# Performance work log

Hardware: AMD Instinct MI355X
Metric: run time of the kernel (lower is better)

The kernel has to match this reference:

```python
import jax, jax.numpy as jnp
import numpy as np

B, H, W, C = 32, 56, 56, 192
P, HEADS = 7, 6
HD = C // HEADS
SCALE = HD ** -0.5
EPS = 1e-5


def _rel_pos_index(p):
    coords = np.stack(np.meshgrid(np.arange(p), np.arange(p), indexing='ij')).reshape(2, -1)
    rel = (coords[:, :, None] - coords[:, None, :]).transpose(1, 2, 0).astype(np.int64)
    rel[:, :, 0] += p - 1
    rel[:, :, 1] += p - 1
    rel[:, :, 0] *= 2 * p - 1
    return rel.sum(-1)  # (p*p, p*p)

REL_IDX = jnp.asarray(_rel_pos_index(P))


def _ln(x, g, b):
    mu = x.mean(-1, keepdims=True)
    var = ((x - mu) ** 2).mean(-1, keepdims=True)
    return (x - mu) * jax.lax.rsqrt(var + EPS) * g + b


def setup_inputs():
    key = jax.random.key(0)
    ks = jax.random.split(key, 8)
    s = 0.02
    return {
        'x': jax.random.normal(ks[0], (B, H * W, C), jnp.float32),
        'norm1_g': jnp.ones((C,), jnp.float32),
        'norm1_b': jnp.zeros((C,), jnp.float32),
        'qkv_w': jax.random.normal(ks[1], (C, 3 * C), jnp.float32) * s,
        'qkv_b': jnp.zeros((3 * C,), jnp.float32),
        'rpe_table': jax.random.normal(ks[2], ((2 * P - 1) ** 2, HEADS), jnp.float32) * s,
        'proj_w': jax.random.normal(ks[3], (C, C), jnp.float32) * s,
        'proj_b': jnp.zeros((C,), jnp.float32),
        'norm2_g': jnp.ones((C,), jnp.float32),
        'norm2_b': jnp.zeros((C,), jnp.float32),
        'fc1_w': jax.random.normal(ks[4], (C, 4 * C), jnp.float32) * s,
        'fc1_b': jnp.zeros((4 * C,), jnp.float32),
        'fc2_w': jax.random.normal(ks[5], (4 * C, C), jnp.float32) * s,
        'fc2_b': jnp.zeros((C,), jnp.float32),
    }


def reference(x, norm1_g, norm1_b, qkv_w, qkv_b, rpe_table, proj_w, proj_b,
              norm2_g, norm2_b, fc1_w, fc1_b, fc2_w, fc2_b):
    N = P * P
    shortcut = x
    h = _ln(x, norm1_g, norm1_b).reshape(B, H, W, C)
    # partition -> (B*nH*nW, N, C)
    h = h.reshape(B, H // P, P, W // P, P, C).transpose(0, 1, 3, 2, 4, 5)
    patches = h.reshape(-1, N, C)
    B_ = patches.shape[0]
    # qkv
    qkv = (patches @ qkv_w + qkv_b).reshape(B_, N, 3, HEADS, HD)
    q, k, v = qkv[:, :, 0], qkv[:, :, 1], qkv[:, :, 2]  # (B_, N, HEADS, HD)
    attn = jnp.einsum('bnhd,bmhd->bhnm', q * SCALE, k)
    bias = rpe_table[REL_IDX.reshape(-1)].reshape(N, N, HEADS).transpose(2, 0, 1)
    attn = jax.nn.softmax(attn + bias[None], axis=-1)
    out = jnp.einsum('bhnm,bmhd->bnhd', attn, v).reshape(B_, N, C)
    out = out @ proj_w + proj_b
    # reverse -> (B, H*W, C)
    out = out.reshape(B, H // P, W // P, P, P, C).transpose(0, 1, 3, 2, 4, 5).reshape(B, H * W, C)
    x = shortcut + out
    h = _ln(x, norm2_g, norm2_b)
    h = jax.nn.gelu(h @ fc1_w + fc1_b, approximate=False) @ fc2_w + fc2_b
    return x + h
```

## Files before the change

### kernel.cpp

```cpp
#include <hip/hip_runtime.h>
#include <cstdint>

using u16 = unsigned short;
using u32 = unsigned int;

typedef __bf16 bf16x8 __attribute__((ext_vector_type(8)));
typedef float f32x4 __attribute__((ext_vector_type(4)));
typedef short short4v __attribute__((ext_vector_type(4)));

constexpr int TOK = 100352;
constexpr float LOG2E = 1.4426950408889634f;
constexpr float SCALE_QL = 0.25503490f;

__device__ __forceinline__ float bf2f(u16 u) {
  union { u32 i; float f; } z; z.i = ((u32)u) << 16; return z.f;
}
__device__ __forceinline__ u16 f2bf(float f) {
  union { float f; u32 i; } z; z.f = f;
  u32 r = z.i + 0x7FFFu + ((z.i >> 16) & 1u);
  return (u16)(r >> 16);
}
__device__ __forceinline__ u32 pk2bf(float a, float b) {
  union { __bf16 h[2]; u32 w; } z;
  z.h[0] = (__bf16)a; z.h[1] = (__bf16)b; return z.w;
}

__device__ __forceinline__ float gelu_f(float v) {
  float u = v * (0.7978845608f + 0.0356774081f * v * v);
  float e = __expf(-2.f * u);
  return v * __builtin_amdgcn_rcpf(1.f + e);
}

__device__ __forceinline__ void gload_lds16(const void* g, void* l) {
  __builtin_amdgcn_global_load_lds((const __attribute__((address_space(1))) void*)g,
                                   (__attribute__((address_space(3))) void*)l, 16, 0, 0);
}

__global__ void transpose_pad(const float* __restrict__ src, u16* __restrict__ dst,
                              int N, int Npad, int K) {
  int id = blockIdx.x * 256 + threadIdx.x;
  if (id >= Npad * K) return;
  int n = id / K, k = id - n * K;
  float v = (n < N) ? src[(size_t)k * N + n] : 0.f;
  dst[id] = f2bf(v);
}

__global__ void transpose_swz1(const float* __restrict__ src, u16* __restrict__ dst) {
  int id = blockIdx.x * 256 + threadIdx.x;
  if (id >= 768 * 192) return;
  int n = id / 192, k = id - n * 192;
  int sg = (k >> 3) ^ (n & 7);
  dst[n * 192 + sg * 8 + (k & 7)] = f2bf(src[(size_t)k * 768 + n]);
}
__global__ void transpose_swz2(const float* __restrict__ src, u16* __restrict__ dst) {
  int id = blockIdx.x * 256 + threadIdx.x;
  if (id >= 192 * 768) return;
  int oc = id / 768, gc = id - oc * 768;
  int ch = gc >> 5, gcl = gc & 31;
  int f = gcl >> 4, gq = (gcl >> 2) & 3, e = gcl & 3;
  int P = oc * 4 + (gq ^ ((oc >> 2) & 3));
  dst[ch * 6144 + P * 8 + f * 4 + e] = f2bf(src[(size_t)gc * 192 + oc]);
}

template<int MODE>
__global__ __launch_bounds__(256) void ln_kernel(const float* __restrict__ x,
                                                 const u16* __restrict__ proj,
                                                 const float* __restrict__ g,
                                                 const float* __restrict__ b,
                                                 u16* __restrict__ out) {
  int row  = blockIdx.x * 4 + (threadIdx.x >> 6);
  int lane = threadIdx.x & 63;
  const float* xr = x + (size_t)row * 192;
  float v[3];
  #pragma unroll
  for (int t = 0; t < 3; ++t) {
    int c = lane + 64 * t;
    v[t] = xr[c];
    if (MODE == 1) v[t] += bf2f(proj[(size_t)row * 192 + c]);
  }
  float s = v[0] + v[1] + v[2];
  #pragma unroll
  for (int o = 32; o; o >>= 1) s += __shfl_xor(s, o);
  float mu = s * (1.f / 192.f);
  float q = 0.f;
  #pragma unroll
  for (int t = 0; t < 3; ++t) { float d = v[t] - mu; q += d * d; }
  #pragma unroll
  for (int o = 32; o; o >>= 1) q += __shfl_xor(q, o);
  float rs = rsqrtf(q * (1.f / 192.f) + 1e-5f);
  #pragma unroll
  for (int t = 0; t < 3; ++t) {
    int c = lane + 64 * t;
    out[(size_t)row * 192 + c] = f2bf((v[t] - mu) * rs * g[c] + b[c]);
  }
}

enum { MQKV = 0, MPROJ = 1 };

template<int MODE, int MT, int NT, int N, int K, int LDC>
__global__ __launch_bounds__(256) void gemm_kernel(
    const u16* __restrict__ A, const u16* __restrict__ BT,
    const float* __restrict__ bias,
    u16* __restrict__ outb)
{
  constexpr int NWG = MT * NT;
  constexpr int NTL = K / 32;
  __shared__ __align__(16) u16 As[3][4096];
  __shared__ __align__(16) u16 Bs[3][4096];
  int tid = threadIdx.x;
  int wg = blockIdx.x;
  int lin = (wg & 7) * (NWG / 8) + (wg >> 3);
  int tileM = (lin / NT) * 128, tileN = (lin % NT) * 128;
  int lane = tid & 63, wave = tid >> 6;
  int wm = wave >> 1, wn = wave & 1;
  int g = lane >> 4, l15 = lane & 15;
  f32x4 acc[4][4] = {};

  int r0 = tid >> 2, kc = (tid & 3) * 8;
  const u16* Arow0 = A  + (size_t)(tileM + r0)      * K + kc;
  const u16* Arow1 = A  + (size_t)(tileM + r0 + 64) * K + kc;
  const u16* Brow0 = BT + (size_t)(tileN + r0)      * K + kc;
  const u16* Brow1 = BT + (size_t)(tileN + r0 + 64) * K + kc;
  const int wo = wave * 512;

#define GSTAGE(buf, k0) do {                              \
    gload_lds16(Arow0 + (k0), &As[buf][wo]);              \
    gload_lds16(Arow1 + (k0), &As[buf][2048 + wo]);       \
    gload_lds16(Brow0 + (k0), &Bs[buf][wo]);              \
    gload_lds16(Brow1 + (k0), &Bs[buf][2048 + wo]);       \
  } while (0)

  GSTAGE(0, 0);
  GSTAGE(1, 32);

  #pragma unroll
  for (int t = 0; t < NTL; ++t) {
    if (t + 1 < NTL) asm volatile("s_waitcnt vmcnt(4)" ::: "memory");
    else             asm volatile("s_waitcnt vmcnt(0)" ::: "memory");
    __builtin_amdgcn_s_barrier();
    __builtin_amdgcn_sched_barrier(0);
    if (t + 2 < NTL) GSTAGE((t + 2) % 3, (t + 2) * 32);
    const int cur = t % 3;
    bf16x8 af[4], bfr[4];
    #pragma unroll
    for (int mi = 0; mi < 4; ++mi)
      af[mi] = *(const bf16x8*)&As[cur][(wm * 64 + mi * 16 + l15) * 32 + g * 8];
    #pragma unroll
    for (int ni = 0; ni < 4; ++ni)
      bfr[ni] = *(const bf16x8*)&Bs[cur][(wn * 64 + ni * 16 + l15) * 32 + g * 8];
    #pragma unroll
    for (int mi = 0; mi < 4; ++mi)
      #pragma unroll
      for (int ni = 0; ni < 4; ++ni)
        acc[mi][ni] = __builtin_amdgcn_mfma_f32_16x16x32_bf16(bfr[ni], af[mi], acc[mi][ni], 0, 0, 0);
    __builtin_amdgcn_sched_barrier(0);
  }
#undef GSTAGE

  int cb = tileN + wn * 64 + g * 4;
  f32x4 bv4[4];
  bool cok[4];
  #pragma unroll
  for (int ni = 0; ni < 4; ++ni) {
    cok[ni] = (cb + ni * 16) < N;
    bv4[ni] = cok[ni] ? *(const f32x4*)&bias[cb + ni * 16] : f32x4{};
  }
  #pragma unroll
  for (int mi = 0; mi < 4; ++mi) {
    size_t row = (size_t)(tileM + wm * 64 + mi * 16 + l15);
    u16* orow = outb + row * LDC + cb;
    #pragma unroll
    for (int ni = 0; ni < 4; ++ni) {
      if (!cok[ni]) continue;
      float v0 = acc[mi][ni][0] + bv4[ni][0];
      float v1 = acc[mi][ni][1] + bv4[ni][1];
      float v2 = acc[mi][ni][2] + bv4[ni][2];
      float v3 = acc[mi][ni][3] + bv4[ni][3];
      if (MODE == MQKV && (cb + ni * 16) < 192) {
        v0 *= SCALE_QL; v1 *= SCALE_QL; v2 *= SCALE_QL; v3 *= SCALE_QL;
      }
      uint2 w;
      w.x = pk2bf(v0, v1);
      w.y = pk2bf(v2, v3);
      *(uint2*)&orow[ni * 16] = w;
    }
  }
}

__global__ __launch_bounds__(256, 3) void mlp_fused(
    const u16* __restrict__ h2, const float* __restrict__ x,
    const u16* __restrict__ projO,
    const u16* __restrict__ w1g,
    const u16* __restrict__ w2g,
    const float* __restrict__ fc1b, const float* __restrict__ fc2b,
    float* __restrict__ out)
{
  __shared__ __align__(16) u16 W1c[2][6144];
  __shared__ __align__(16) u16 W2c[2][6144];
  __shared__ float B1s[768];
  __shared__ float B2s[192];

  int tid = threadIdx.x, lane = tid & 63, wave = tid >> 6;
  int g = lane >> 4, l15 = lane & 15;
  size_t row = (size_t)blockIdx.x * 64 + wave * 16 + l15;

  for (int c = tid; c < 768; c += 256) B1s[c] = fc1b[c];
  if (tid < 192) B2s[tid] = fc2b[tid];

  bf16x8 xf[6];
  #pragma unroll
  for (int ks = 0; ks < 6; ++ks)
    xf[ks] = *(const bf16x8*)&h2[row * 192 + ks * 32 + g * 8];

#define MSTAGE(c) do {                                                    \
    _Pragma("unroll")                                                     \
    for (int it = 0; it < 3; ++it) {                                      \
      int s = it * 256 + tid;                                             \
      gload_lds16(w1g + (size_t)(c) * 6144 + s * 8,                       \
                  &W1c[(c) & 1][(it * 256 + wave * 64) * 8]);             \
      gload_lds16(w2g + (size_t)(c) * 6144 + s * 8,                       \
                  &W2c[(c) & 1][(it * 256 + wave * 64) * 8]);             \
    }                                                                     \
  } while (0)

  MSTAGE(0);
  __syncthreads();

  f32x4 accO[12] = {};
  const int p2sw = g ^ ((l15 >> 2) & 3);

  #pragma unroll 2
  for (int c = 0; c < 24; ++c) {
    asm volatile("s_waitcnt vmcnt(0)" ::: "memory");
    __builtin_amdgcn_s_barrier();
    __builtin_amdgcn_sched_barrier(0);
    if (c + 1 < 24) MSTAGE(c + 1);
    const int bs = c & 1;

    f32x4 acc1[2] = {};
    #pragma unroll
    for (int ks = 0; ks < 6; ++ks) {
      #pragma unroll
      for (int f = 0; f < 2; ++f) {
        int rl = f * 16 + l15;
        int sg = (ks * 4 + g) ^ (rl & 7);
        bf16x8 wf = *(const bf16x8*)&W1c[bs][rl * 192 + sg * 8];
        acc1[f] = __builtin_amdgcn_mfma_f32_16x16x32_bf16(wf, xf[ks], acc1[f], 0, 0, 0);
      }
    }
    short4v bp[2];
    #pragma unroll
    for (int f = 0; f < 2; ++f) {
      f32x4 bv = *(const f32x4*)&B1s[c * 32 + f * 16 + g * 4];
      float p0 = gelu_f(acc1[f][0] + bv[0]);
      float p1 = gelu_f(acc1[f][1] + bv[1]);
      float p2 = gelu_f(acc1[f][2] + bv[2]);
      float p3 = gelu_f(acc1[f][3] + bv[3]);
      union { u32 w[2]; short4v v; } uu;
      uu.w[0] = pk2bf(p0, p1);
      uu.w[1] = pk2bf(p2, p3);
      bp[f] = uu.v;
    }
    #pragma unroll
    for (int n = 0; n < 12; ++n) {
      int oc = n * 16 + l15;
      int P = oc * 4 + p2sw;
      union { bf16x8 v8; short4v h[2]; } wu;
      wu.v8 = *(const bf16x8*)&W2c[bs][P * 8];
      accO[n] = __builtin_amdgcn_mfma_f32_16x16x16bf16_1k(wu.h[0], bp[0], accO[n], 0, 0, 0);
      accO[n] = __builtin_amdgcn_mfma_f32_16x16x16bf16_1k(wu.h[1], bp[1], accO[n], 0, 0, 0);
    }
    __builtin_amdgcn_sched_barrier(0);
  }
#undef MSTAGE

  const float* xrow = x + row * 192;
  const u16*  prow = projO + row * 192;
  float*      orow = out + row * 192;
  #pragma unroll
  for (int n = 0; n < 12; ++n) {
    int cb = n * 16 + g * 4;
    f32x4 bv = *(const f32x4*)&B2s[cb];
    f32x4 xv = *(const f32x4*)&xrow[cb];
    uint2 pv = *(const uint2*)&prow[cb];
    f32x4 o;
    o[0] = accO[n][0] + bv[0] + xv[0] + bf2f((u16)(pv.x & 0xffff));
    o[1] = accO[n][1] + bv[1] + xv[1] + bf2f((u16)(pv.x >> 16));
    o[2] = accO[n][2] + bv[2] + xv[2] + bf2f((u16)(pv.y & 0xffff));
    o[3] = accO[n][3] + bv[3] + xv[3] + bf2f((u16)(pv.y >> 16));
    *(f32x4*)&orow[cb] = o;
  }
}

__global__ __launch_bounds__(384, 4) void attn_kernel(const u16* __restrict__ qkv,
                                                      const float* __restrict__ rpe,
                                                      u16* __restrict__ aout) {
  __shared__ __align__(16) u16 VT[192 * 72];
  __shared__ float RPE[1014];

  int tid = threadIdx.x;
  int win = blockIdx.x;
  int b = win >> 6, rem = win & 63, wh = rem >> 3, ww = rem & 7;
  const size_t wbase = (size_t)b * 3136 + (size_t)(wh * 7) * 56 + ww * 7;

  for (int c = tid; c < 1176; c += 384) {
    int dchunk = c / 49, tkn = c - dchunk * 49;
    int d0 = dchunk * 8;
    int yi = tkn / 7, xi = tkn - yi * 7;
    size_t t = wbase + yi * 56 + xi;
    uint4 v = *(const uint4*)&qkv[t * 576 + 384 + d0];
    const u16* e = (const u16*)&v;
    #pragma unroll
    for (int u = 0; u < 8; ++u) VT[(d0 + u) * 72 + tkn] = e[u];
  }
  for (int c = tid; c < 2880; c += 384) {
    int d = c / 15, n = 49 + (c - d * 15);
    VT[d * 72 + n] = 0;
  }
  for (int c = tid; c < 1014; c += 384) RPE[c] = rpe[c] * LOG2E;
  __syncthreads();

  int wave = tid >> 6, lane = tid & 63;
  int g = lane >> 4, l15 = lane & 15;
  int h = wave;

  bf16x8 afk[4], bfq[4];
  #pragma unroll
  for (int f = 0; f < 4; ++f) {
    int row = f * 16 + l15; row = min(row, 48);
    int y = row / 7, xx = row - y * 7;
    const u16* base = &qkv[(wbase + (size_t)y * 56 + xx) * 576];
    bfq[f] = *(const bf16x8*)(base + h * 32 + g * 8);
    afk[f] = *(const bf16x8*)(base + 192 + h * 32 + g * 8);
  }

  f32x4 acc[4][4] = {};
  __builtin_amdgcn_s_setprio(1);
  #pragma unroll
  for (int mj = 0; mj < 4; ++mj)
    #pragma unroll
    for (int ni = 0; ni < 4; ++ni)
      acc[mj][ni] = __builtin_amdgcn_mfma_f32_16x16x32_bf16(afk[mj], bfq[ni], acc[mj][ni], 0, 0, 0);
  __builtin_amdgcn_s_setprio(0);

  float sums[4];
  short4v bp[4][4];
  #pragma unroll
  for (int ni = 0; ni < 4; ++ni) {
    int i = ni * 16 + l15;
    int yi = i / 7, xi = i - yi * 7;
    #pragma unroll
    for (int mj = 0; mj < 4; ++mj)
      #pragma unroll
      for (int r = 0; r < 4; ++r) {
        int j = mj * 16 + g * 4 + r;
        int yj = j / 7, xj = j - yj * 7;
        int idx = (yi - yj + 6) * 13 + (xi - xj + 6);
        idx = max(0, min(idx, 168));
        float s = acc[mj][ni][r] + RPE[idx * 6 + h];
        acc[mj][ni][r] = (j < 49) ? s : -1e30f;
      }
    float m = -1e30f;
    #pragma unroll
    for (int mj = 0; mj < 4; ++mj) {
      f32x4 a = acc[mj][ni];
      m = fmaxf(m, fmaxf(fmaxf(a[0], a[1]), fmaxf(a[2], a[3])));
    }
    m = fmaxf(m, __shfl_xor(m, 16));
    m = fmaxf(m, __shfl_xor(m, 32));
    float sum = 0.f;
    #pragma unroll
    for (int mj = 0; mj < 4; ++mj) {
      float p0 = exp2f(acc[mj][ni][0] - m);
      float p1 = exp2f(acc[mj][ni][1] - m);
      float p2 = exp2f(acc[mj][ni][2] - m);
      float p3 = exp2f(acc[mj][ni][3] - m);
      sum += (p0 + p1) + (p2 + p3);
      union { u32 w[2]; short4v v; } uu;
      uu.w[0] = pk2bf(p0, p1);
      uu.w[1] = pk2bf(p2, p3);
      bp[ni][mj] = uu.v;
    }
    sum += __shfl_xor(sum, 16);
    sum += __shfl_xor(sum, 32);
    sums[ni] = sum;
  }

  f32x4 accO[2][4] = {};
  #pragma unroll
  for (int ks = 0; ks < 4; ++ks) {
    short4v av[2];
    #pragma unroll
    for (int md = 0; md < 2; ++md)
      av[md] = *(const short4v*)&VT[(h * 32 + md * 16 + l15) * 72 + ks * 16 + g * 4];
    __builtin_amdgcn_s_setprio(1);
    #pragma unroll
    for (int md = 0; md < 2; ++md)
      #pragma unroll
      for (int ni = 0; ni < 4; ++ni)
        accO[md][ni] = __builtin_amdgcn_mfma_f32_16x16x16bf16_1k(av[md], bp[ni][ks], accO[md][ni], 0, 0, 0);
    __builtin_amdgcn_s_setprio(0);
  }

  #pragma unroll
  for (int ni = 0; ni < 4; ++ni) {
    int i = ni * 16 + l15;
    if (i >= 49) continue;
    float inv = __builtin_amdgcn_rcpf(sums[ni]);
    int y = i / 7, xx = i - y * 7;
    u16* orow = &aout[(wbase + (size_t)y * 56 + xx) * 192 + h * 32];
    #pragma unroll
    for (int md = 0; md < 2; ++md) {
      int d0 = md * 16 + g * 4;
      *(u32*)&orow[d0]     = pk2bf(accO[md][ni][0] * inv, accO[md][ni][1] * inv);
      *(u32*)&orow[d0 + 2] = pk2bf(accO[md][ni][2] * inv, accO[md][ni][3] * inv);
    }
  }
}

extern "C" void kernel_launch(void* const* d_in, const int* in_sizes, int n_in,
                              void* d_out, int out_size, void* d_ws, size_t ws_size,
                              hipStream_t stream) {
  const float* x      = (const float*)d_in[0];
  const float* n1g    = (const float*)d_in[1];
  const float* n1b    = (const float*)d_in[2];
  const float* qkv_w  = (const float*)d_in[3];
  const float* qkv_b  = (const float*)d_in[4];
  const float* rpe    = (const float*)d_in[5];
  const float* proj_w = (const float*)d_in[6];
  const float* proj_b = (const float*)d_in[7];
  const float* n2g    = (const float*)d_in[8];
  const float* n2b    = (const float*)d_in[9];
  const float* fc1_w  = (const float*)d_in[10];
  const float* fc1_b  = (const float*)d_in[11];
  const float* fc2_w  = (const float*)d_in[12];
  const float* fc2_b  = (const float*)d_in[13];
  float* out = (float*)d_out;
  char* ws = (char*)d_ws;

  u16* qkvT  = (u16*)(ws + 0);
  u16* projT = (u16*)(ws + 245760);
  u16* fc1T  = (u16*)(ws + 344064);
  u16* fc2T  = (u16*)(ws + 638976);
  u16* ln1   = (u16*)(ws + 1048576);
  u16* qkvB  = (u16*)(ws + 39583744);
  u16* projO = (u16*)(ws + 155189248);
  u16* attnO = ln1;
  u16* h2    = qkvB;
  if (ws_size < 193724416u) return;

  transpose_pad<<<(640*192+255)/256, 256, 0, stream>>>(qkv_w,  qkvT, 576, 640, 192);
  transpose_pad<<<(256*192+255)/256, 256, 0, stream>>>(proj_w, projT, 192, 256, 192);
  transpose_swz1<<<576, 256, 0, stream>>>(fc1_w, fc1T);
  transpose_swz2<<<576, 256, 0, stream>>>(fc2_w, fc2T);

  ln_kernel<0><<<TOK/4, 256, 0, stream>>>(x, nullptr, n1g, n1b, ln1);

  gemm_kernel<MQKV, 784, 5, 576, 192, 576><<<3920, 256, 0, stream>>>(
      ln1, qkvT, qkv_b, qkvB);

  attn_kernel<<<2048, 384, 0, stream>>>(qkvB, rpe, attnO);

  gemm_kernel<MPROJ, 784, 2, 192, 192, 192><<<1568, 256, 0, stream>>>(
      attnO, projT, proj_b, projO);

  ln_kernel<1><<<TOK/4, 256, 0, stream>>>(x, projO, n2g, n2b, h2);

  mlp_fused<<<TOK/64, 256, 0, stream>>>(
      h2, x, projO, fc1T, fc2T, fc1_b, fc2_b, out);
}
```

Baseline: 345.8 us.

## Double rows per wave in fused MLP to reuse staged weights; fold GELU into exp2

Each wave in the fused MLP kernel now processes two 16-row tiles, so every W1/W2 fragment read from LDS feeds two MFMAs. The grid is halved and launch bounds drop to 2 blocks per SM. The aim is to halve weight staging traffic and LDS reads per token. The cost is doubled accumulator registers and lower occupancy. GELU now folds the constants so it can call exp2f directly.

```diff
diff --git a/kernel.cpp b/kernel.cpp
--- a/kernel.cpp
+++ b/kernel.cpp
@@ -26,8 +26,8 @@
 }
 
 __device__ __forceinline__ float gelu_f(float v) {
-  float u = v * (0.7978845608f + 0.0356774081f * v * v);
-  float e = __expf(-2.f * u);
+  float t = -v * (2.3022587f + 0.10294455f * v * v);
+  float e = exp2f(t);
   return v * __builtin_amdgcn_rcpf(1.f + e);
 }
 
@@ -187,7 +187,7 @@
   }
 }
 
-__global__ __launch_bounds__(256, 3) void mlp_fused(
+__global__ __launch_bounds__(256, 2) void mlp_fused(
     const u16* __restrict__ h2, const float* __restrict__ x,
     const u16* __restrict__ projO,
     const u16* __restrict__ w1g,
@@ -202,15 +202,17 @@
 
   int tid = threadIdx.x, lane = tid & 63, wave = tid >> 6;
   int g = lane >> 4, l15 = lane & 15;
-  size_t row = (size_t)blockIdx.x * 64 + wave * 16 + l15;
+  size_t rowA = (size_t)blockIdx.x * 128 + wave * 32 + l15;
 
   for (int c = tid; c < 768; c += 256) B1s[c] = fc1b[c];
   if (tid < 192) B2s[tid] = fc2b[tid];
 
-  bf16x8 xf[6];
-  #pragma unroll
-  for (int ks = 0; ks < 6; ++ks)
-    xf[ks] = *(const bf16x8*)&h2[row * 192 + ks * 32 + g * 8];
+  bf16x8 xfA[6], xfB[6];
+  #pragma unroll
+  for (int ks = 0; ks < 6; ++ks) {
+    xfA[ks] = *(const bf16x8*)&h2[rowA * 192 + ks * 32 + g * 8];
+    xfB[ks] = *(const bf16x8*)&h2[(rowA + 16) * 192 + ks * 32 + g * 8];
+  }
 
 #define MSTAGE(c) do {                                                    \
     _Pragma("unroll")                                                     \
@@ -226,7 +228,8 @@
   MSTAGE(0);
   __syncthreads();
 
-  f32x4 accO[12] = {};
+  f32x4 accOA[12] = {};
+  f32x4 accOB[12] = {};
   const int p2sw = g ^ ((l15 >> 2) & 3);
 
   #pragma unroll 2
@@ -237,7 +240,7 @@
     if (c + 1 < 24) MSTAGE(c + 1);
     const int bs = c & 1;
 
-    f32x4 acc1[2] = {};
+    f32x4 acc1A[2] = {}, acc1B[2] = {};
     #pragma unroll
     for (int ks = 0; ks < 6; ++ks) {
       #pragma unroll
@@ -245,21 +248,34 @@
         int rl = f * 16 + l15;
         int sg = (ks * 4 + g) ^ (rl & 7);
         bf16x8 wf = *(const bf16x8*)&W1c[bs][rl * 192 + sg * 8];
-        acc1[f] = __builtin_amdgcn_mfma_f32_16x16x32_bf16(wf, xf[ks], acc1[f], 0, 0, 0);
+        acc1A[f] = __builtin_amdgcn_mfma_f32_16x16x32_bf16(wf, xfA[ks], acc1A[f], 0, 0, 0);
+        acc1B[f] = __builtin_amdgcn_mfma_f32_16x16x32_bf16(wf, xfB[ks], acc1B[f], 0, 0, 0);
       }
     }
-    short4v bp[2];
+    short4v bpA[2], bpB[2];
     #pragma unroll
     for (int f = 0; f < 2; ++f) {
       f32x4 bv = *(const f32x4*)&B1s[c * 32 + f * 16 + g * 4];
-      float p0 = gelu_f(acc1[f][0] + bv[0]);
-      float p1 = gelu_f(acc1[f][1] + bv[1]);
-      float p2 = gelu_f(acc1[f][2] + bv[2]);
-      float p3 = gelu_f(acc1[f][3] + bv[3]);
-      union { u32 w[2]; short4v v; } uu;
-      uu.w[0] = pk2bf(p0, p1);
-      uu.w[1] = pk2bf(p2, p3);
-      bp[f] = uu.v;
+      {
+        float p0 = gelu_f(acc1A[f][0] + bv[0]);
+        float p1 = gelu_f(acc1A[f][1] + bv[1]);
+        float p2 = gelu_f(acc1A[f][2] + bv[2]);
+        float p3 = gelu_f(acc1A[f][3] + bv[3]);
+        union { u32 w[2]; short4v v; } uu;
+        uu.w[0] = pk2bf(p0, p1);
+        uu.w[1] = pk2bf(p2, p3);
+        bpA[f] = uu.v;
+      }
+      {
+        float p0 = gelu_f(acc1B[f][0] + bv[0]);
+        float p1 = gelu_f(acc1B[f][1] + bv[1]);
+        float p2 = gelu_f(acc1B[f][2] + bv[2]);
+        float p3 = gelu_f(acc1B[f][3] + bv[3]);
+        union { u32 w[2]; short4v v; } uu;
+        uu.w[0] = pk2bf(p0, p1);
+        uu.w[1] = pk2bf(p2, p3);
+        bpB[f] = uu.v;
+      }
     }
     #pragma unroll
     for (int n = 0; n < 12; ++n) {
@@ -267,28 +283,35 @@
       int P = oc * 4 + p2sw;
       union { bf16x8 v8; short4v h[2]; } wu;
       wu.v8 = *(const bf16x8*)&W2c[bs][P * 8];
-      accO[n] = __builtin_amdgcn_mfma_f32_16x16x16bf16_1k(wu.h[0], bp[0], accO[n], 0, 0, 0);
-      accO[n] = __builtin_amdgcn_mfma_f32_16x16x16bf16_1k(wu.h[1], bp[1], accO[n], 0, 0, 0);
+      accOA[n] = __builtin_amdgcn_mfma_f32_16x16x16bf16_1k(wu.h[0], bpA[0], accOA[n], 0, 0, 0);
+      accOA[n] = __builtin_amdgcn_mfma_f32_16x16x16bf16_1k(wu.h[1], bpA[1], accOA[n], 0, 0, 0);
+      accOB[n] = __builtin_amdgcn_mfma_f32_16x16x16bf16_1k(wu.h[0], bpB[0], accOB[n], 0, 0, 0);
+      accOB[n] = __builtin_amdgcn_mfma_f32_16x16x16bf16_1k(wu.h[1], bpB[1], accOB[n], 0, 0, 0);
     }
     __builtin_amdgcn_sched_barrier(0);
   }
 #undef MSTAGE
 
-  const float* xrow = x + row * 192;
-  const u16*  prow = projO + row * 192;
-  float*      orow = out + row * 192;
-  #pragma unroll
-  for (int n = 0; n < 12; ++n) {
-    int cb = n * 16 + g * 4;
-    f32x4 bv = *(const f32x4*)&B2s[cb];
-    f32x4 xv = *(const f32x4*)&xrow[cb];
-    uint2 pv = *(const uint2*)&prow[cb];
-    f32x4 o;
-    o[0] = accO[n][0] + bv[0] + xv[0] + bf2f((u16)(pv.x & 0xffff));
-    o[1] = accO[n][1] + bv[1] + xv[1] + bf2f((u16)(pv.x >> 16));
-    o[2] = accO[n][2] + bv[2] + xv[2] + bf2f((u16)(pv.y & 0xffff));
-    o[3] = accO[n][3] + bv[3] + xv[3] + bf2f((u16)(pv.y >> 16));
-    *(f32x4*)&orow[cb] = o;
+  #pragma unroll
+  for (int half = 0; half < 2; ++half) {
+    size_t row = rowA + half * 16;
+    const f32x4* accO = half ? accOB : accOA;
+    const float* xrow = x + row * 192;
+    const u16*  prow = projO + row * 192;
+    float*      orow = out + row * 192;
+    #pragma unroll
+    for (int n = 0; n < 12; ++n) {
+      int cb = n * 16 + g * 4;
+      f32x4 bv = *(const f32x4*)&B2s[cb];
+      f32x4 xv = *(const f32x4*)&xrow[cb];
+      uint2 pv = *(const uint2*)&prow[cb];
+      f32x4 o;
+      o[0] = accO[n][0] + bv[0] + xv[0] + bf2f((u16)(pv.x & 0xffff));
+      o[1] = accO[n][1] + bv[1] + xv[1] + bf2f((u16)(pv.x >> 16));
+      o[2] = accO[n][2] + bv[2] + xv[2] + bf2f((u16)(pv.y & 0xffff));
+      o[3] = accO[n][3] + bv[3] + xv[3] + bf2f((u16)(pv.y >> 16));
+      *(f32x4*)&orow[cb] = o;
+    }
   }
 }
 
@@ -466,6 +489,6 @@
 
   ln_kernel<1><<<TOK/4, 256, 0, stream>>>(x, projO, n2g, n2b, h2);
 
-  mlp_fused<<<TOK/64, 256, 0, stream>>>(
+  mlp_fused<<<TOK/128, 256, 0, stream>>>(
       h2, x, projO, fc1T, fc2T, fc1_b, fc2_b, out);
 }
```

Measured after the change: 354.9 us. 1.03x slower.

## Fuse projection GEMM with residual add and LayerNorm2 into one kernel

Applied to the files above, without the earlier changes.

Replaces the separate projection GEMM and second LayerNorm kernels with one kernel. Each block computes a full 128x192 output row tile, adds bias and the residual, writes the fp32 residual, and computes LayerNorm statistics in registers before emitting bf16 h2. The MLP epilogue then reads the precomputed residual instead of x plus the bf16 projection output, which drops a launch and a round trip of the projection result. It also folds log2e into the GELU exponent so exp2f can be used. Risks are fewer workgroups (784) with high register pressure, and single-pass variance that is less numerically stable.

```diff
diff --git a/kernel.cpp b/kernel.cpp
--- a/kernel.cpp
+++ b/kernel.cpp
@@ -26,8 +26,8 @@
 }
 
 __device__ __forceinline__ float gelu_f(float v) {
-  float u = v * (0.7978845608f + 0.0356774081f * v * v);
-  float e = __expf(-2.f * u);
+  float t = -v * (2.3022587f + 0.10294455f * v * v);
+  float e = exp2f(t);
   return v * __builtin_amdgcn_rcpf(1.f + e);
 }
 
@@ -95,7 +95,7 @@
   }
 }
 
-enum { MQKV = 0, MPROJ = 1 };
+enum { MQKV = 0 };
 
 template<int MODE, int MT, int NT, int N, int K, int LDC>
 __global__ __launch_bounds__(256) void gemm_kernel(
@@ -187,9 +187,119 @@
   }
 }
 
+__global__ __launch_bounds__(256, 2) void proj_ln(
+    const u16* __restrict__ A,
+    const u16* __restrict__ BT,
+    const float* __restrict__ bias,
+    const float* __restrict__ x,
+    const float* __restrict__ n2g, const float* __restrict__ n2b,
+    float* __restrict__ resid, u16* __restrict__ h2)
+{
+  constexpr int NWG = 784;
+  __shared__ __align__(16) u16 As[3][4096];
+  __shared__ __align__(16) u16 Bs[3][6144];
+  int tid = threadIdx.x;
+  int wg = blockIdx.x;
+  int lin = (wg & 7) * (NWG / 8) + (wg >> 3);
+  int tileM = lin * 128;
+  int lane = tid & 63, wave = tid >> 6;
+  int g = lane >> 4, l15 = lane & 15;
+  f32x4 acc[2][12] = {};
+
+  int r0 = tid >> 2, kc = (tid & 3) * 8;
+  const u16* Arow0 = A + (size_t)(tileM + r0)      * 192 + kc;
+  const u16* Arow1 = A + (size_t)(tileM + r0 + 64) * 192 + kc;
+  const u16* Brow[3];
+  #pragma unroll
+  for (int i = 0; i < 3; ++i) {
+    int s = (wave * 3 + i) * 64 + lane;
+    Brow[i] = BT + (size_t)(s >> 2) * 192 + (s & 3) * 8;
+  }
+  const int wo = wave * 512;
+
+#define PSTAGE(buf, k0) do {                                   \
+    gload_lds16(Arow0 + (k0), &As[buf][wo]);                   \
+    gload_lds16(Arow1 + (k0), &As[buf][2048 + wo]);            \
+    _Pragma("unroll")                                          \
+    for (int i = 0; i < 3; ++i)                                \
+      gload_lds16(Brow[i] + (k0), &Bs[buf][(wave * 3 + i) * 512]); \
+  } while (0)
+
+  PSTAGE(0, 0);
+  PSTAGE(1, 32);
+
+  #pragma unroll
+  for (int t = 0; t < 6; ++t) {
+    if (t + 1 < 6) asm volatile("s_waitcnt vmcnt(5)" ::: "memory");
+    else           asm volatile("s_waitcnt vmcnt(0)" ::: "memory");
+    __builtin_amdgcn_s_barrier();
+    __builtin_amdgcn_sched_barrier(0);
+    if (t + 2 < 6) PSTAGE((t + 2) % 3, (t + 2) * 32);
+    const int cur = t % 3;
+    bf16x8 af[2], bfr[12];
+    #pragma unroll
+    for (int mi = 0; mi < 2; ++mi)
+      af[mi] = *(const bf16x8*)&As[cur][(wave * 32 + mi * 16 + l15) * 32 + g * 8];
+    #pragma unroll
+    for (int ni = 0; ni < 12; ++ni)
+      bfr[ni] = *(const bf16x8*)&Bs[cur][(ni * 16 + l15) * 32 + g * 8];
+    #pragma unroll
+    for (int mi = 0; mi < 2; ++mi)
+      #pragma unroll
+      for (int ni = 0; ni < 12; ++ni)
+        acc[mi][ni] = __builtin_amdgcn_mfma_f32_16x16x32_bf16(bfr[ni], af[mi], acc[mi][ni], 0, 0, 0);
+    __builtin_amdgcn_sched_barrier(0);
+  }
+#undef PSTAGE
+
+  float s1[2] = {0.f, 0.f}, s2[2] = {0.f, 0.f};
+  #pragma unroll
+  for (int mi = 0; mi < 2; ++mi) {
+    size_t row = (size_t)(tileM + wave * 32 + mi * 16 + l15);
+    #pragma unroll
+    for (int ni = 0; ni < 12; ++ni) {
+      int cb = ni * 16 + g * 4;
+      f32x4 bv = *(const f32x4*)&bias[cb];
+      f32x4 xv = *(const f32x4*)&x[row * 192 + cb];
+      f32x4 o;
+      #pragma unroll
+      for (int r = 0; r < 4; ++r) {
+        o[r] = acc[mi][ni][r] + bv[r] + xv[r];
+        s1[mi] += o[r];
+        s2[mi] += o[r] * o[r];
+      }
+      acc[mi][ni] = o;
+      *(f32x4*)&resid[row * 192 + cb] = o;
+    }
+  }
+  #pragma unroll
+  for (int mi = 0; mi < 2; ++mi) {
+    s1[mi] += __shfl_xor(s1[mi], 16); s1[mi] += __shfl_xor(s1[mi], 32);
+    s2[mi] += __shfl_xor(s2[mi], 16); s2[mi] += __shfl_xor(s2[mi], 32);
+  }
+  #pragma unroll
+  for (int mi = 0; mi < 2; ++mi) {
+    float mu = s1[mi] * (1.f / 192.f);
+    float var = s2[mi] * (1.f / 192.f) - mu * mu;
+    float rs = rsqrtf(var + 1e-5f);
+    size_t row = (size_t)(tileM + wave * 32 + mi * 16 + l15);
+    #pragma unroll
+    for (int ni = 0; ni < 12; ++ni) {
+      int cb = ni * 16 + g * 4;
+      f32x4 gv = *(const f32x4*)&n2g[cb];
+      f32x4 bv = *(const f32x4*)&n2b[cb];
+      uint2 w;
+      w.x = pk2bf((acc[mi][ni][0] - mu) * rs * gv[0] + bv[0],
+                  (acc[mi][ni][1] - mu) * rs * gv[1] + bv[1]);
+      w.y = pk2bf((acc[mi][ni][2] - mu) * rs * gv[2] + bv[2],
+                  (acc[mi][ni][3] - mu) * rs * gv[3] + bv[3]);
+      *(uint2*)&h2[row * 192 + cb] = w;
+    }
+  }
+}
+
 __global__ __launch_bounds__(256, 3) void mlp_fused(
-    const u16* __restrict__ h2, const float* __restrict__ x,
-    const u16* __restrict__ projO,
+    const u16* __restrict__ h2, const float* __restrict__ resid,
     const u16* __restrict__ w1g,
     const u16* __restrict__ w2g,
     const float* __restrict__ fc1b, const float* __restrict__ fc2b,
@@ -274,20 +384,18 @@
   }
 #undef MSTAGE
 
-  const float* xrow = x + row * 192;
-  const u16*  prow = projO + row * 192;
+  const float* rrow = resid + row * 192;
   float*      orow = out + row * 192;
   #pragma unroll
   for (int n = 0; n < 12; ++n) {
     int cb = n * 16 + g * 4;
     f32x4 bv = *(const f32x4*)&B2s[cb];
-    f32x4 xv = *(const f32x4*)&xrow[cb];
-    uint2 pv = *(const uint2*)&prow[cb];
+    f32x4 rv = *(const f32x4*)&rrow[cb];
     f32x4 o;
-    o[0] = accO[n][0] + bv[0] + xv[0] + bf2f((u16)(pv.x & 0xffff));
-    o[1] = accO[n][1] + bv[1] + xv[1] + bf2f((u16)(pv.x >> 16));
-    o[2] = accO[n][2] + bv[2] + xv[2] + bf2f((u16)(pv.y & 0xffff));
-    o[3] = accO[n][3] + bv[3] + xv[3] + bf2f((u16)(pv.y >> 16));
+    o[0] = accO[n][0] + bv[0] + rv[0];
+    o[1] = accO[n][1] + bv[1] + rv[1];
+    o[2] = accO[n][2] + bv[2] + rv[2];
+    o[3] = accO[n][3] + bv[3] + rv[3];
     *(f32x4*)&orow[cb] = o;
   }
 }
@@ -444,7 +552,7 @@
   u16* fc2T  = (u16*)(ws + 638976);
   u16* ln1   = (u16*)(ws + 1048576);
   u16* qkvB  = (u16*)(ws + 39583744);
-  u16* projO = (u16*)(ws + 155189248);
+  float* resid = (float*)(ws + 78118912);
   u16* attnO = ln1;
   u16* h2    = qkvB;
   if (ws_size < 193724416u) return;
@@ -461,11 +569,9 @@
 
   attn_kernel<<<2048, 384, 0, stream>>>(qkvB, rpe, attnO);
 
-  gemm_kernel<MPROJ, 784, 2, 192, 192, 192><<<1568, 256, 0, stream>>>(
-      attnO, projT, proj_b, projO);
-
-  ln_kernel<1><<<TOK/4, 256, 0, stream>>>(x, projO, n2g, n2b, h2);
+  proj_ln<<<784, 256, 0, stream>>>(
+      attnO, projT, proj_b, x, n2g, n2b, resid, h2);
 
   mlp_fused<<<TOK/64, 256, 0, stream>>>(
-      h2, x, projO, fc1T, fc2T, fc1_b, fc2_b, out);
-}
+      h2, resid, fc1T, fc2T, fc1_b, fc2_b, out);
+}
```

New measurement: 340.1 us. No clear change (-1.7%).
